# Performance work log

Measured on AMD Instinct MI355X. Metric: run time of the kernel, lower is better.

Reference implementation:

```python
import jax, jax.numpy as jnp
import numpy as np

EPS = 1e-5
K_NBR = 21   # num_neighbors + 1 (self)
PSI = 4


def _bn(x, g, b):
    # BatchNorm (training-mode forward): channel-last, normalize over all other axes
    axes = tuple(range(x.ndim - 1))
    m = jnp.mean(x, axis=axes, keepdims=True)
    v = jnp.var(x, axis=axes, keepdims=True)
    return (x - m) * jax.lax.rsqrt(v + EPS) * g + b


def setup_inputs() -> dict:
    key = jax.random.key(0)
    ks = jax.random.split(key, 16)
    B, N, Cin, Cout = 4, 2048, 64, 256
    h = Cout // 2
    w_ch = Cout // PSI
    heads = 2 * PSI - 1

    def w(k, o, i):
        return jax.random.normal(k, (o, i), dtype=jnp.float32) * (1.0 / np.sqrt(i))

    p = {}
    p['xyz'] = jax.random.normal(ks[0], (B, N, 3), dtype=jnp.float32)
    p['f'] = jax.random.normal(ks[1], (B, Cin, N), dtype=jnp.float32)
    p['W_geo'] = w(ks[2], h, 6);       p['g_geo'] = jnp.ones(h);   p['b_geo'] = jnp.zeros(h)
    p['W_feat'] = w(ks[3], h, 2 * Cin); p['g_feat'] = jnp.ones(h); p['b_feat'] = jnp.zeros(h)
    p['g_bn'] = jnp.ones(Cout); p['b_bn'] = jnp.zeros(Cout)
    p['W_q'] = w(ks[4], Cout, Cout); p['g_q'] = jnp.ones(Cout); p['b_q'] = jnp.zeros(Cout)
    p['W_k'] = w(ks[5], Cout, Cout); p['g_k'] = jnp.ones(Cout); p['b_k'] = jnp.zeros(Cout)
    p['W_v'] = w(ks[6], Cout, Cout); p['g_v'] = jnp.ones(Cout); p['b_v'] = jnp.zeros(Cout)
    p['W_fus'] = w(ks[7], Cout, heads * w_ch); p['bias_fus'] = jnp.zeros(Cout)
    p['g_fus'] = jnp.ones(Cout); p['b_fus'] = jnp.zeros(Cout)
    p['g_ln'] = jnp.ones(Cout); p['b_ln'] = jnp.zeros(Cout)
    p['W_mlp'] = w(ks[8], Cout, Cout); p['bias_mlp'] = jnp.zeros(Cout)
    return p


def reference(xyz, f, W_geo, g_geo, b_geo, W_feat, g_feat, b_feat, g_bn, b_bn,
              W_q, g_q, b_q, W_k, g_k, b_k, W_v, g_v, b_v,
              W_fus, bias_fus, g_fus, b_fus, g_ln, b_ln, W_mlp, bias_mlp):
    B, N, _ = xyz.shape
    Cout = g_bn.shape[0]
    w_ch = Cout // PSI
    d_sh = w_ch // 2
    heads = 2 * PSI - 1

    # ---- PositionFusion: KNN grouping ----
    sq = jnp.sum(xyz * xyz, axis=-1)                                   # [B,N]
    d2 = sq[:, :, None] + sq[:, None, :] - 2.0 * jnp.einsum('bnd,bmd->bnm', xyz, xyz)
    _, idx = jax.lax.top_k(-d2, K_NBR)                                 # [B,N,K]

    grouped_xyz = jax.vmap(lambda p, i: p[i])(xyz, idx)                # [B,N,K,3]
    xyz_diff = grouped_xyz - xyz[:, :, None, :]
    geo_in = jnp.concatenate(
        [jnp.broadcast_to(xyz[:, :, None, :], grouped_xyz.shape), xyz_diff], axis=-1)  # [B,N,K,6]

    ft = jnp.transpose(f, (0, 2, 1))                                   # [B,N,Cin]
    grouped_f = jax.vmap(lambda p, i: p[i])(ft, idx)                   # [B,N,K,Cin]
    feat_in = jnp.concatenate(
        [grouped_f, jnp.broadcast_to(ft[:, :, None, :], grouped_f.shape)], axis=-1)    # [B,N,K,2Cin]

    geo = jax.nn.relu(_bn(jnp.einsum('bnki,oi->bnko', geo_in, W_geo), g_geo, b_geo))
    fea = jax.nn.relu(_bn(jnp.einsum('bnki,oi->bnko', feat_in, W_feat), g_feat, b_feat))
    feature_ = jnp.max(jnp.concatenate([geo, fea], axis=-1), axis=2)   # [B,N,Cout] (maxpool over K)

    # ---- BatchNorm1d ----
    x = _bn(feature_, g_bn, b_bn)

    # ---- Shifted-channel multi-head attention ----
    q = jax.nn.relu(_bn(jnp.einsum('bnc,oc->bno', x, W_q), g_q, b_q))
    k = jax.nn.relu(_bn(jnp.einsum('bnc,oc->bno', x, W_k), g_k, b_k))
    v = jax.nn.relu(_bn(jnp.einsum('bnc,oc->bno', x, W_v), g_v, b_v))

    qh = jnp.stack([q[..., m * d_sh:m * d_sh + w_ch] for m in range(heads)], axis=1)  # [B,H,N,w]
    kh = jnp.stack([k[..., m * d_sh:m * d_sh + w_ch] for m in range(heads)], axis=1)
    vh = jnp.stack([v[..., m * d_sh:m * d_sh + w_ch] for m in range(heads)], axis=1)

    a = jax.nn.softmax(jnp.einsum('bhnc,bhmc->bhnm', qh, kh), axis=-1)  # [B,H,N,N]
    o = jnp.einsum('bhnm,bhmc->bhnc', a, vh)                            # [B,H,N,w]
    O = jnp.transpose(o, (0, 2, 1, 3)).reshape(B, N, heads * w_ch)      # channel-concat per head

    fus = jax.nn.relu(_bn(jnp.einsum('bnc,oc->bno', O, W_fus) + bias_fus, g_fus, b_fus))

    feature__ = fus + feature_                                          # residual

    # ---- LayerNorm over channels ----
    m = jnp.mean(feature__, axis=-1, keepdims=True)
    var = jnp.var(feature__, axis=-1, keepdims=True)
    y = (feature__ - m) * jax.lax.rsqrt(var + EPS) * g_ln + b_ln

    out = feature__ + (jnp.einsum('bnc,oc->bno', y, W_mlp) + bias_mlp)
    return jnp.transpose(out, (0, 2, 1))                                # [B,Cout,N] like torch
```

## Files before the change

kernel.cpp:

```cpp
#include <hip/hip_runtime.h>
#include <math.h>

#define NB    4
#define NPTS  2048
#define ROWS  (NB*NPTS)
#define CIN   64
#define COUT  256
#define KNBR  21
#define NHEADS 7
#define WCH   64
#define DSH   32
#define LOG2E 1.4426950408889634f

typedef __attribute__((ext_vector_type(8))) short short8;
typedef __attribute__((ext_vector_type(4))) float floatx4;

#if __has_builtin(__builtin_amdgcn_exp2f)
#define EXP2(x) __builtin_amdgcn_exp2f(x)
#else
#define EXP2(x) __expf((x)*0.6931471805599453f)
#endif
#if __has_builtin(__builtin_amdgcn_rcpf)
#define RCP(x) __builtin_amdgcn_rcpf(x)
#else
#define RCP(x) (1.0f/(x))
#endif

__device__ __forceinline__ ushort f2bf(float x) {
    unsigned u = __float_as_uint(x);
    u += 0x7fffu + ((u >> 16) & 1u);
    return (ushort)(u >> 16);
}

template<int N>
__device__ __forceinline__ float dpp_ror16(float x) {
    return __int_as_float(__builtin_amdgcn_update_dpp(
        0, __float_as_int(x), 0x120 | N, 0xF, 0xF, true));
}
__device__ __forceinline__ float dpp_max16(float x) {
    x = fmaxf(x, dpp_ror16<1>(x));
    x = fmaxf(x, dpp_ror16<2>(x));
    x = fmaxf(x, dpp_ror16<4>(x));
    x = fmaxf(x, dpp_ror16<8>(x));
    return x;
}
__device__ __forceinline__ float dpp_sum16(float x) {
    x += dpp_ror16<1>(x);
    x += dpp_ror16<2>(x);
    x += dpp_ror16<4>(x);
    x += dpp_ror16<8>(x);
    return x;
}

template<int CTRL, int RMASK>
__device__ __forceinline__ unsigned dpp_umin_step(unsigned x) {
    unsigned t = (unsigned)__builtin_amdgcn_update_dpp((int)x, (int)x, CTRL, RMASK, 0xF, false);
    return (t < x) ? t : x;
}
__device__ __forceinline__ unsigned wave_min_u32(unsigned x) {
    x = dpp_umin_step<0x111, 0xF>(x);
    x = dpp_umin_step<0x112, 0xF>(x);
    x = dpp_umin_step<0x114, 0xF>(x);
    x = dpp_umin_step<0x118, 0xF>(x);
    x = dpp_umin_step<0x142, 0xA>(x);
    x = dpp_umin_step<0x143, 0xC>(x);
    return (unsigned)__builtin_amdgcn_readlane((int)x, 63);
}

__global__ __launch_bounds__(256) void prep_knn(const float* __restrict__ f, const float* __restrict__ Wf,
                                                const float* __restrict__ xyz, const float* __restrict__ Wg,
                                                const float* __restrict__ W_q, const float* __restrict__ W_k,
                                                const float* __restrict__ W_v, const float* __restrict__ W_fus,
                                                float* __restrict__ X, float* __restrict__ A,
                                                ushort* __restrict__ Wb, float* __restrict__ sums,
                                                int* __restrict__ idx) {
    __shared__ float4 SXQ[2048];
    int t = threadIdx.x;
    int blk = blockIdx.x;
    if (blk < 512) {
        float* As = (float*)SXQ;
        float* Ws = As + 16*68;
        int bx = blk & 127, by = blk >> 7;
        if (by == 0 && bx < 12) sums[bx*256 + t] = 0.f;
        int gid = (by*128 + bx)*256 + t;
        for (int i = gid; i < 311296; i += 131072) {
            const float* Wsrc; int off;
            if (i < 65536)       { Wsrc = W_q;   off = i; }
            else if (i < 131072) { Wsrc = W_k;   off = i - 65536; }
            else if (i < 196608) { Wsrc = W_v;   off = i - 131072; }
            else                 { Wsrc = W_fus; off = i - 196608; }
            Wb[i] = f2bf(Wsrc[off]);
        }
        int r0 = bx * 64, n0 = by * 64;
        for (int e = t; e < 4096; e += 256) {
            int row = r0 + (e >> 6), c = n0 + (e & 63), cc = c & 127;
            float x = xyz[row*3], y = xyz[row*3+1], z = xyz[row*3+2];
            const float* w = Wg + cc*6;
            float s = (c < 128) ? ((w[3]*x + w[4]*y) + w[5]*z)
                                : (((w[0]-w[3])*x + (w[1]-w[4])*y) + (w[2]-w[5])*z);
            A[(size_t)row*256 + c] = s;
        }
        int b = r0 >> 11, nbase = r0 & 2047;
        int tx = t & 15, ty = t >> 4;
        float acc[4][4];
#pragma unroll
        for (int i = 0; i < 4; i++)
#pragma unroll
            for (int j = 0; j < 4; j++) acc[i][j] = 0.f;
        int m64 = t & 63, kg = t >> 6;
        int lk = t & 15, lm = t >> 4;
        for (int k0 = 0; k0 < 64; k0 += 16) {
#pragma unroll
            for (int p = 0; p < 4; p++) {
                int k = kg*4 + p;
                As[k*68 + m64] = f[(size_t)b*CIN*NPTS + (size_t)(k0 + k)*NPTS + nbase + m64];
            }
#pragma unroll
            for (int i2 = 0; i2 < 4; i2++) {
                int cg = n0 + lm + 16*i2;
                Ws[lk*68 + lm + 16*i2] = Wf[(size_t)(cg & 127)*128 + (cg >> 7)*64 + k0 + lk];
            }
            __syncthreads();
#pragma unroll
            for (int kq = 0; kq < 16; kq++) {
                float4 a  = *(const float4*)&As[kq*68 + 4*ty];
                float4 b4 = *(const float4*)&Ws[kq*68 + 4*tx];
                float av[4] = {a.x, a.y, a.z, a.w};
                float bv[4] = {b4.x, b4.y, b4.z, b4.w};
#pragma unroll
                for (int i = 0; i < 4; i++)
#pragma unroll
                    for (int j = 0; j < 4; j++) acc[i][j] = fmaf(av[i], bv[j], acc[i][j]);
            }
            __syncthreads();
        }
#pragma unroll
        for (int i = 0; i < 4; i++)
#pragma unroll
            for (int j = 0; j < 4; j++)
                X[(size_t)(r0 + 4*ty + i)*256 + n0 + 4*tx + j] = acc[i][j];
        return;
    }
    int kb = blk - 512;
    int b = kb >> 9;
    int g = kb & 511;
    for (int m = t; m < NPTS; m += 256) {
        float x = xyz[(size_t)b*NPTS*3 + m*3];
        float y = xyz[(size_t)b*NPTS*3 + m*3 + 1];
        float z = xyz[(size_t)b*NPTS*3 + m*3 + 2];
        SXQ[m] = make_float4(x, y, z, (x*x + y*y) + z*z);
    }
    __syncthreads();
    int w = t >> 6, lane = t & 63;
    int n = g*4 + w;
    float4 q4 = SXQ[n];
    float qx = q4.x, qy = q4.y, qz = q4.z, sqn = q4.w;
    unsigned key[32];
#pragma unroll
    for (int i = 0; i < 32; i++) {
        int m = lane + (i << 6);
        float4 p = SXQ[m];
        float dt = (qx*p.x + qy*p.y) + qz*p.z;
        float d2 = fmaxf((sqn + p.w) - 2.0f*dt, 0.f);
        key[i] = (__float_as_uint(d2) & 0xFFFFF800u) | (unsigned)m;
    }
    unsigned winkey = 0xFFFFFFFFu;
    for (int kk = 0; kk < 32; kk++) {
        unsigned lv = key[0];
#pragma unroll
        for (int i = 1; i < 32; i++) lv = (key[i] < lv) ? key[i] : lv;
        unsigned win = wave_min_u32(lv);
        if (lane == kk) winkey = win;
        unsigned widx = win & 2047u;
        int slot = (int)(widx >> 6);
        bool own = (lane == (int)(widx & 63u));
#pragma unroll
        for (int i = 0; i < 32; i++)
            if (i == slot && own) key[i] = 0xFFFFFFFFu;
    }
    double d2r;
    int mr;
    {
        double qx64 = (double)qx, qy64 = (double)qy, qz64 = (double)qz;
        double sqn64 = qx64*qx64 + qy64*qy64 + qz64*qz64;
        if (lane < 32) {
            mr = (int)(winkey & 2047u);
            float4 p = SXQ[mr];
            double x = (double)p.x, y = (double)p.y, z = (double)p.z;
            double sqm = x*x + y*y + z*z;
            double dt  = qx64*x + qy64*y + qz64*z;
            d2r = (sqn64 + sqm) - 2.0*dt;
        } else {
            d2r = INFINITY; mr = 0x7FFFFFFF;
        }
    }
#pragma unroll
    for (int k = 2; k <= 32; k <<= 1) {
#pragma unroll
        for (int j = k >> 1; j > 0; j >>= 1) {
            double od = __shfl_xor(d2r, j, 64);
            int    om = __shfl_xor(mr, j, 64);
            bool up    = ((lane & k) == 0);
            bool lower = ((lane & j) == 0);
            bool oless = (od < d2r) || (od == d2r && om < mr);
            bool keepOther = up ? (lower ? oless : !oless) : (lower ? !oless : oless);
            if (keepOther) { d2r = od; mr = om; }
        }
    }
    if (lane < KNBR)
        idx[((size_t)b*NPTS + n)*KNBR + lane] = mr;
}

__global__ __launch_bounds__(256) void stats_gf(const float* __restrict__ geoBC, const float* __restrict__ featAC,
                                                const int* __restrict__ idx, const float* __restrict__ g_geo,
                                                const float* __restrict__ g_feat,
                                                float* __restrict__ sums, float* __restrict__ xsel) {
    int c = threadIdx.x;
    int cc = c & 127;
    const float* base = (c < 128) ? geoBC : featAC;
    bool wantmax = ((c < 128) ? g_geo[cc] : g_feat[cc]) >= 0.f;
    float s = 0.f, ss = 0.f;
    int r0 = blockIdx.x * 32;
    for (int r = r0; r < r0 + 32; r++) {
        int b = r >> 11;
        float ctr = base[(size_t)r*256 + 128 + cc];
        float mx = -1e30f, mn = 1e30f;
        const int* ip = idx + (size_t)r*KNBR;
        for (int kk = 0; kk < KNBR; kk++) {
            int j = ip[kk];
            float xv = ctr + base[((size_t)(b*NPTS + j))*256 + cc];
            mx = fmaxf(mx, xv); mn = fminf(mn, xv);
            s += xv; ss += xv*xv;
        }
        xsel[(size_t)r*256 + c] = wantmax ? mx : mn;
    }
    atomicAdd(&sums[c], s);
    atomicAdd(&sums[256 + c], ss);
}

__global__ __launch_bounds__(256) void feature_maxsel(const float* __restrict__ xsel, const float* __restrict__ sums,
                                                      const float* __restrict__ g_geo, const float* __restrict__ b_geo,
                                                      const float* __restrict__ g_feat, const float* __restrict__ b_feat,
                                                      float* __restrict__ feat, float* __restrict__ sums_bn1) {
    int c = threadIdx.x;
    const float inv = 1.0f / (float)(ROWS*KNBR);
    float mean = sums[c]*inv;
    float var  = sums[256+c]*inv - mean*mean;
    float g  = (c < 128) ? g_geo[c] : g_feat[c-128];
    float bb = (c < 128) ? b_geo[c] : b_feat[c-128];
    float sc = g / sqrtf(var + 1e-5f);
    float tt = bb - mean*sc;
    float s = 0.f, ss = 0.f;
    int r0 = blockIdx.x*32;
    for (int r = r0; r < r0+32; r++) {
        size_t i = (size_t)r*256 + c;
        float y = fmaxf(fmaf(sc, xsel[i], tt), 0.f);
        feat[i] = y; s += y; ss += y*y;
    }
    atomicAdd(&sums_bn1[c], s); atomicAdd(&sums_bn1[256+c], ss);
}

__global__ __launch_bounds__(256) void gemm_qkv(const float* __restrict__ Af, const float* __restrict__ sums_in,
                                                const float* __restrict__ g_bn, const float* __restrict__ b_bn,
                                                const ushort* __restrict__ Wb,
                                                float* __restrict__ QKVF, float* __restrict__ sums) {
    __shared__ float bns[2][256];
    __shared__ float red[4][256][2];
    int t = threadIdx.x;
    int r0 = blockIdx.x * 64, g = blockIdx.y;
    int w = t >> 6, lane = t & 63;
    int r15 = lane & 15, quad = lane >> 4;
    {
        float mean = sums_in[512 + t] * (1.0f/(float)ROWS);
        float var  = sums_in[768 + t] * (1.0f/(float)ROWS) - mean*mean;
        float sc = g_bn[t] / sqrtf(var + 1e-5f);
        bns[0][t] = sc;
        bns[1][t] = b_bn[t] - mean*sc;
    }
    __syncthreads();
    short8 aq[8];
    {
        const float* ap = Af + (size_t)(r0 + 16*w + r15)*256;
#pragma unroll
        for (int kc = 0; kc < 8; kc++) {
            int k0 = 32*kc + 8*quad;
            float4 a0 = *(const float4*)&ap[k0];
            float4 a1 = *(const float4*)&ap[k0+4];
            float4 s0 = *(const float4*)&bns[0][k0];
            float4 s1 = *(const float4*)&bns[0][k0+4];
            float4 h0 = *(const float4*)&bns[1][k0];
            float4 h1 = *(const float4*)&bns[1][k0+4];
            ushort u8[8];
            u8[0] = f2bf(fmaf(s0.x, a0.x, h0.x)); u8[1] = f2bf(fmaf(s0.y, a0.y, h0.y));
            u8[2] = f2bf(fmaf(s0.z, a0.z, h0.z)); u8[3] = f2bf(fmaf(s0.w, a0.w, h0.w));
            u8[4] = f2bf(fmaf(s1.x, a1.x, h1.x)); u8[5] = f2bf(fmaf(s1.y, a1.y, h1.y));
            u8[6] = f2bf(fmaf(s1.z, a1.z, h1.z)); u8[7] = f2bf(fmaf(s1.w, a1.w, h1.w));
            aq[kc] = *(short8*)u8;
        }
    }
    floatx4 zero4 = {0.f, 0.f, 0.f, 0.f};
    floatx4 acc[16];
#pragma unroll
    for (int st = 0; st < 16; st++) acc[st] = zero4;
    const ushort* wbase = Wb + (size_t)g*65536 + (size_t)r15*256 + 8*quad;
#pragma unroll
    for (int st = 0; st < 16; st++) {
        const ushort* wp = wbase + (size_t)(16*st)*256;
#pragma unroll
        for (int kc = 0; kc < 8; kc++) {
            short8 bf = *(const short8*)(wp + 32*kc);
            acc[st] = __builtin_amdgcn_mfma_f32_16x16x32_bf16(aq[kc], bf, acc[st], 0, 0, 0);
        }
    }
#pragma unroll
    for (int st = 0; st < 16; st++) {
        float s  = (acc[st][0] + acc[st][1]) + (acc[st][2] + acc[st][3]);
        float q2 = (acc[st][0]*acc[st][0] + acc[st][1]*acc[st][1]) +
                   (acc[st][2]*acc[st][2] + acc[st][3]*acc[st][3]);
        s  += __shfl_xor(s, 16, 64);  s  += __shfl_xor(s, 32, 64);
        q2 += __shfl_xor(q2, 16, 64); q2 += __shfl_xor(q2, 32, 64);
        if (lane < 16) { red[w][16*st + r15][0] = s; red[w][16*st + r15][1] = q2; }
#pragma unroll
        for (int reg = 0; reg < 4; reg++)
            QKVF[(size_t)(r0 + 16*w + 4*quad + reg)*768 + g*256 + 16*st + r15] = acc[st][reg];
    }
    __syncthreads();
    {
        float s = red[0][t][0] + red[1][t][0] + red[2][t][0] + red[3][t][0];
        float q = red[0][t][1] + red[1][t][1] + red[2][t][1] + red[3][t][1];
        atomicAdd(&sums[1024 + g*512 + t], s);
        atomicAdd(&sums[1024 + g*512 + 256 + t], q);
    }
}

__global__ __launch_bounds__(256) void affine_qkv(const float* __restrict__ QKVF, const float* __restrict__ sums,
                                                  const float* __restrict__ g_q, const float* __restrict__ b_q,
                                                  const float* __restrict__ g_k, const float* __restrict__ b_k,
                                                  const float* __restrict__ g_v, const float* __restrict__ b_v,
                                                  ushort* __restrict__ qk, ushort* __restrict__ vt) {
    __shared__ float sts[6][256];
    __shared__ ushort tile[64][72];
    int t = threadIdx.x;
    {
        const float* gs[3] = {g_q, g_k, g_v};
        const float* bs[3] = {b_q, b_k, b_v};
#pragma unroll
        for (int g = 0; g < 3; g++) {
            float mean = sums[1024 + g*512 + t] * (1.0f/(float)ROWS);
            float var  = sums[1024 + g*512 + 256 + t] * (1.0f/(float)ROWS) - mean*mean;
            float sc = gs[g][t] / sqrtf(var + 1e-5f);
            float sh = bs[g][t] - mean*sc;
            if (g == 0) { sc *= LOG2E; sh *= LOG2E; }
            sts[2*g][t] = sc;
            sts[2*g+1][t] = sh;
        }
    }
    __syncthreads();
    int r0 = blockIdx.x * 64, c0 = blockIdx.y * 64;
    int b = r0 >> 11, nbase = r0 & 2047;
    if (c0 < 512) {
#pragma unroll
        for (int rep = 0; rep < 16; rep++) {
            int e = t + 256*rep;
            int row = e >> 6, c = e & 63;
            int col = c0 + c, g = col >> 8, cc = col & 255;
            float v = QKVF[(size_t)(r0 + row)*768 + col];
            v = fmaxf(fmaf(sts[2*g][cc], v, sts[2*g+1][cc]), 0.f);
            qk[(size_t)(r0 + row)*512 + col] = f2bf(v);
        }
    } else {
#pragma unroll
        for (int rep = 0; rep < 16; rep++) {
            int e = t + 256*rep;
            int row = e >> 6, c = e & 63;
            int col = c0 + c, cc = col & 255;
            float v = QKVF[(size_t)(r0 + row)*768 + col];
            v = fmaxf(fmaf(sts[4][cc], v, sts[5][cc]), 0.f);
            tile[c][row] = f2bf(v);
        }
        __syncthreads();
#pragma unroll
        for (int rep = 0; rep < 16; rep++) {
            int e = t + 256*rep;
            int cc = e >> 6, nn = e & 63;
            vt[((size_t)(b*256 + (c0 - 512) + cc))*2048 + nbase + nn] = tile[cc][nn];
        }
    }
}

__global__ __launch_bounds__(256) void attn2(const ushort* __restrict__ qk, const ushort* __restrict__ vt,
                                             float* __restrict__ obuf) {
    __shared__ ushort Ksh[64*72];
    __shared__ ushort Vts[64*72];
    __shared__ ushort Psh[128*72];
    int h = blockIdx.y, b = blockIdx.z;
    int r0 = blockIdx.x * 128;
    int t = threadIdx.x;
    int w = t >> 6, lane = t & 63;
    int r15 = lane & 15, quad = lane >> 4;
    size_t rowbase = (size_t)b*NPTS;
    int hoff = h*DSH;

    short8 aq[2][2];
#pragma unroll
    for (int u = 0; u < 2; u++)
#pragma unroll
        for (int s = 0; s < 2; s++)
            aq[u][s] = *(const short8*)(qk + (rowbase + r0 + 64*u + 16*w + r15)*512 + hoff + 32*s + 8*quad);

    floatx4 zero4 = {0.f, 0.f, 0.f, 0.f};
    floatx4 oacc[2][4];
    float mrun[2][4], lrun[2][4];
#pragma unroll
    for (int u = 0; u < 2; u++)
#pragma unroll
        for (int i = 0; i < 4; i++) { oacc[u][i] = zero4; mrun[u][i] = -1e30f; lrun[u][i] = 0.f; }

    for (int m0 = 0; m0 < NPTS; m0 += 64) {
#pragma unroll
        for (int rep = 0; rep < 2; rep++) {
            int e = t + 256*rep;
            int rr = e >> 3, c = e & 7;
            *(uint4*)&Ksh[rr*72 + 8*c] =
                *(const uint4*)(qk + (rowbase + m0 + rr)*512 + 256 + hoff + 8*c);
            *(uint4*)&Vts[rr*72 + 8*c] =
                *(const uint4*)(vt + ((size_t)(b*256 + hoff + rr))*2048 + m0 + 8*c);
        }
        __syncthreads();

        floatx4 sacc[2][4];
#pragma unroll
        for (int u = 0; u < 2; u++)
#pragma unroll
            for (int tt = 0; tt < 4; tt++) sacc[u][tt] = zero4;
#pragma unroll
        for (int tt = 0; tt < 4; tt++) {
            int key = 16*tt + r15;
#pragma unroll
            for (int s = 0; s < 2; s++) {
                short8 kf = *(const short8*)&Ksh[key*72 + 32*s + 8*quad];
#pragma unroll
                for (int u = 0; u < 2; u++)
                    sacc[u][tt] = __builtin_amdgcn_mfma_f32_16x16x32_bf16(aq[u][s], kf, sacc[u][tt], 0, 0, 0);
            }
        }

        float pm[2][4][4];
#pragma unroll
        for (int u = 0; u < 2; u++)
#pragma unroll
            for (int reg = 0; reg < 4; reg++) {
                float rmax = fmaxf(fmaxf(sacc[u][0][reg], sacc[u][1][reg]),
                                   fmaxf(sacc[u][2][reg], sacc[u][3][reg]));
                rmax = dpp_max16(rmax);
                float mnew = fmaxf(mrun[u][reg], rmax);
                float alpha = EXP2(mrun[u][reg] - mnew);
                float rs = 0.f;
#pragma unroll
                for (int tt = 0; tt < 4; tt++) {
                    float p = EXP2(sacc[u][tt][reg] - mnew);
                    pm[u][tt][reg] = p; rs += p;
                }
                rs = dpp_sum16(rs);
                lrun[u][reg] = lrun[u][reg]*alpha + rs;
                mrun[u][reg] = mnew;
#pragma unroll
                for (int td = 0; td < 4; td++) oacc[u][td][reg] *= alpha;
            }

#pragma unroll
        for (int u = 0; u < 2; u++)
#pragma unroll
            for (int reg = 0; reg < 4; reg++) {
                int row = 64*u + 16*w + 4*quad + reg;
#pragma unroll
                for (int tt = 0; tt < 4; tt++)
                    Psh[row*72 + 16*tt + r15] = f2bf(pm[u][tt][reg]);
            }
        __syncthreads();

#pragma unroll
        for (int s = 0; s < 2; s++) {
            short8 pf[2];
#pragma unroll
            for (int u = 0; u < 2; u++)
                pf[u] = *(const short8*)&Psh[(64*u + 16*w + r15)*72 + 32*s + 8*quad];
#pragma unroll
            for (int td = 0; td < 4; td++) {
                short8 vf = *(const short8*)&Vts[(16*td + r15)*72 + 32*s + 8*quad];
#pragma unroll
                for (int u = 0; u < 2; u++)
                    oacc[u][td] = __builtin_amdgcn_mfma_f32_16x16x32_bf16(pf[u], vf, oacc[u][td], 0, 0, 0);
            }
        }
        __syncthreads();
    }

#pragma unroll
    for (int u = 0; u < 2; u++)
#pragma unroll
        for (int reg = 0; reg < 4; reg++) {
            int grow = r0 + 64*u + 16*w + 4*quad + reg;
            float invl = RCP(lrun[u][reg]);
#pragma unroll
            for (int td = 0; td < 4; td++)
                obuf[(rowbase + grow)*(size_t)(NHEADS*WCH) + h*WCH + 16*td + r15] = oacc[u][td][reg]*invl;
        }
}

__global__ __launch_bounds__(256) void gemm_fus(const float* __restrict__ OBUF, const ushort* __restrict__ Wb,
                                                const float* __restrict__ bias, float* __restrict__ C,
                                                float* __restrict__ sums) {
    __shared__ float red[4][128][2];
    int t = threadIdx.x;
    int r0 = blockIdx.x * 64, n0 = blockIdx.y * 128;
    int w = t >> 6, lane = t & 63;
    int r15 = lane & 15, quad = lane >> 4;
    int arow = 16*w + r15;
    short8 aq[14];
    {
        const float* p0 = OBUF + (size_t)(r0 + arow)*448;
#pragma unroll
        for (int kc = 0; kc < 14; kc++) {
            int k0 = 32*kc + 8*quad;
            float4 x0 = *(const float4*)&p0[k0];
            float4 y0 = *(const float4*)&p0[k0+4];
            ushort u8[8];
            u8[0] = f2bf(x0.x); u8[1] = f2bf(x0.y);
            u8[2] = f2bf(x0.z); u8[3] = f2bf(x0.w);
            u8[4] = f2bf(y0.x); u8[5] = f2bf(y0.y);
            u8[6] = f2bf(y0.z); u8[7] = f2bf(y0.w);
            aq[kc] = *(short8*)u8;
        }
    }
    floatx4 zero4 = {0.f, 0.f, 0.f, 0.f};
    floatx4 acc[8];
#pragma unroll
    for (int st = 0; st < 8; st++) acc[st] = zero4;
    const ushort* wbase = Wb + 196608 + (size_t)(n0 + r15)*448 + 8*quad;
#pragma unroll
    for (int st = 0; st < 8; st++) {
        const ushort* wp = wbase + (size_t)(16*st)*448;
#pragma unroll
        for (int kc = 0; kc < 14; kc++) {
            short8 bf = *(const short8*)(wp + 32*kc);
            acc[st] = __builtin_amdgcn_mfma_f32_16x16x32_bf16(aq[kc], bf, acc[st], 0, 0, 0);
        }
    }
#pragma unroll
    for (int st = 0; st < 8; st++) {
        int col = n0 + 16*st + r15;
        float bi = bias[col];
        float v0 = acc[st][0] + bi, v1 = acc[st][1] + bi, v2 = acc[st][2] + bi, v3 = acc[st][3] + bi;
        float s  = (v0 + v1) + (v2 + v3);
        float q2 = (v0*v0 + v1*v1) + (v2*v2 + v3*v3);
        s  += __shfl_xor(s, 16, 64);  s  += __shfl_xor(s, 32, 64);
        q2 += __shfl_xor(q2, 16, 64); q2 += __shfl_xor(q2, 32, 64);
        if (lane < 16) { red[w][16*st + r15][0] = s; red[w][16*st + r15][1] = q2; }
        C[(size_t)(r0 + 16*w + 4*quad + 0)*256 + col] = v0;
        C[(size_t)(r0 + 16*w + 4*quad + 1)*256 + col] = v1;
        C[(size_t)(r0 + 16*w + 4*quad + 2)*256 + col] = v2;
        C[(size_t)(r0 + 16*w + 4*quad + 3)*256 + col] = v3;
    }
    __syncthreads();
    {
        int col = t >> 1, which = t & 1;
        float v = red[0][col][which] + red[1][col][which] + red[2][col][which] + red[3][col][which];
        atomicAdd(&sums[2560 + which*256 + n0 + col], v);
    }
}

__global__ __launch_bounds__(256) void gemm_mlp_ln(const float* __restrict__ FUSP, const float* __restrict__ A,
                                                   const float* __restrict__ sums,
                                                   const float* __restrict__ g_fus, const float* __restrict__ b_fus,
                                                   const float* __restrict__ g_ln, const float* __restrict__ b_ln,
                                                   const float* __restrict__ W, const float* __restrict__ bias,
                                                   float* __restrict__ outp) {
    __shared__ float Ys[256][68];
    __shared__ float FFs[64][65];
    __shared__ float Ws[16][68];
    __shared__ float tr[64][65];
    __shared__ float SC[256], SH[256], GL[256], BL[256];
    int t = threadIdx.x;
    int r0 = blockIdx.x*64, n0 = blockIdx.y*64;
    {
        float mean0 = sums[2560 + t] * (1.0f/(float)ROWS);
        float var0  = sums[2560 + 256 + t] * (1.0f/(float)ROWS) - mean0*mean0;
        float sc = g_fus[t] / sqrtf(var0 + 1e-5f);
        SC[t] = sc; SH[t] = b_fus[t] - mean0*sc;
        GL[t] = g_ln[t]; BL[t] = b_ln[t];
    }
    __syncthreads();
    int row = t >> 2, seg = t & 3;
    size_t rb = (size_t)(r0 + row)*256;
    float4 vv[16];
    float s = 0.f, ss = 0.f;
#pragma unroll
    for (int j = 0; j < 16; j++) {
        int c = seg*64 + 4*j;
        float4 fp = *(const float4*)&FUSP[rb + c];
        float4 fe = *(const float4*)&A[rb + c];
        float4 sc4 = *(const float4*)&SC[c];
        float4 sh4 = *(const float4*)&SH[c];
        float4 v;
        v.x = fmaxf(fmaf(sc4.x, fp.x, sh4.x), 0.f) + fe.x;
        v.y = fmaxf(fmaf(sc4.y, fp.y, sh4.y), 0.f) + fe.y;
        v.z = fmaxf(fmaf(sc4.z, fp.z, sh4.z), 0.f) + fe.z;
        v.w = fmaxf(fmaf(sc4.w, fp.w, sh4.w), 0.f) + fe.w;
        vv[j] = v;
        s  += (v.x + v.y) + (v.z + v.w);
        ss += (v.x*v.x + v.y*v.y) + (v.z*v.z + v.w*v.w);
        if (seg == blockIdx.y) *(float4*)&FFs[row][4*j] = v;
    }
    s  += __shfl_xor(s, 1, 64);  s  += __shfl_xor(s, 2, 64);
    ss += __shfl_xor(ss, 1, 64); ss += __shfl_xor(ss, 2, 64);
    float mean = s * (1.f/256.f);
    float var  = ss * (1.f/256.f) - mean*mean;
    float rin  = 1.f/sqrtf(var + 1e-5f);
#pragma unroll
    for (int j = 0; j < 16; j++) {
        int c = seg*64 + 4*j;
        float4 gl = *(const float4*)&GL[c];
        float4 bl = *(const float4*)&BL[c];
        float4 v = vv[j];
        Ys[c+0][row] = (v.x - mean)*rin*gl.x + bl.x;
        Ys[c+1][row] = (v.y - mean)*rin*gl.y + bl.y;
        Ys[c+2][row] = (v.z - mean)*rin*gl.z + bl.z;
        Ys[c+3][row] = (v.w - mean)*rin*gl.w + bl.w;
    }
    __syncthreads();
    int tx = t & 15, ty = t >> 4;
    int lk = t & 15, lm = t >> 4;
    float acc[4][4];
#pragma unroll
    for (int i = 0; i < 4; i++)
#pragma unroll
        for (int j = 0; j < 4; j++) acc[i][j] = 0.f;
    for (int k0 = 0; k0 < 256; k0 += 16) {
#pragma unroll
        for (int i2 = 0; i2 < 4; i2++)
            Ws[lk][lm + 16*i2] = W[(size_t)(n0 + lm + 16*i2)*256 + k0 + lk];
        __syncthreads();
#pragma unroll
        for (int kq = 0; kq < 16; kq++) {
            float4 a  = *(const float4*)&Ys[k0 + kq][4*ty];
            float4 b4 = *(const float4*)&Ws[kq][4*tx];
            float av[4] = {a.x, a.y, a.z, a.w};
            float bv[4] = {b4.x, b4.y, b4.z, b4.w};
#pragma unroll
            for (int i = 0; i < 4; i++)
#pragma unroll
                for (int j = 0; j < 4; j++) acc[i][j] = fmaf(av[i], bv[j], acc[i][j]);
        }
        __syncthreads();
    }
#pragma unroll
    for (int i = 0; i < 4; i++)
#pragma unroll
        for (int j = 0; j < 4; j++) {
            float v = acc[i][j] + bias[n0 + 4*tx + j] + FFs[4*ty + i][4*tx + j];
            tr[4*tx + j][4*ty + i] = v;
        }
    __syncthreads();
    int b = r0 >> 11, nbase = r0 & 2047;
#pragma unroll
    for (int rep = 0; rep < 16; rep++) {
        int e = t + 256*rep;
        int cl = e >> 6, nl = e & 63;
        outp[((size_t)(b*256 + n0 + cl))*2048 + nbase + nl] = tr[cl][nl];
    }
}

extern "C" void kernel_launch(void* const* d_in, const int* in_sizes, int n_in,
                              void* d_out, int out_size, void* d_ws, size_t ws_size,
                              hipStream_t stream) {
    const float* xyz    = (const float*)d_in[0];
    const float* f      = (const float*)d_in[1];
    const float* W_geo  = (const float*)d_in[2];
    const float* g_geo  = (const float*)d_in[3];
    const float* b_geo  = (const float*)d_in[4];
    const float* W_feat = (const float*)d_in[5];
    const float* g_feat = (const float*)d_in[6];
    const float* b_feat = (const float*)d_in[7];
    const float* g_bn   = (const float*)d_in[8];
    const float* b_bn   = (const float*)d_in[9];
    const float* W_q    = (const float*)d_in[10];
    const float* g_q    = (const float*)d_in[11];
    const float* b_q    = (const float*)d_in[12];
    const float* W_k    = (const float*)d_in[13];
    const float* g_k    = (const float*)d_in[14];
    const float* b_k    = (const float*)d_in[15];
    const float* W_v    = (const float*)d_in[16];
    const float* g_v    = (const float*)d_in[17];
    const float* b_v    = (const float*)d_in[18];
    const float* W_fus  = (const float*)d_in[19];
    const float* bias_fus = (const float*)d_in[20];
    const float* g_fus  = (const float*)d_in[21];
    const float* b_fus  = (const float*)d_in[22];
    const float* g_ln   = (const float*)d_in[23];
    const float* b_ln   = (const float*)d_in[24];
    const float* W_mlp  = (const float*)d_in[25];
    const float* bias_mlp = (const float*)d_in[26];

    float* ws = (float*)d_ws;
    const size_t MBF = 262144;
    float* SUMS  = ws;
    int*   IDX   = (int*)(ws + 16384);
    float* A     = ws + 1*MBF;
    float* X     = ws + 9*MBF;
    ushort* QK16 = (ushort*)(ws + 9*MBF);
    float* FUSP  = ws + 9*MBF;
    float* CSEL  = ws + 17*MBF;
    float* QKVF  = ws + 17*MBF;
    float* OBUF  = ws + 17*MBF;
    ushort* VT16 = (ushort*)(ws + 45*MBF);
    ushort* WB16 = (ushort*)(ws + 49*MBF);

    prep_knn<<<2560, 256, 0, stream>>>(f, W_feat, xyz, W_geo, W_q, W_k, W_v, W_fus,
                                       X, A, WB16, SUMS, IDX);
    stats_gf<<<256, 256, 0, stream>>>(A, X, IDX, g_geo, g_feat, SUMS, CSEL);
    feature_maxsel<<<256, 256, 0, stream>>>(CSEL, SUMS, g_geo, b_geo, g_feat, b_feat, A, SUMS + 512);
    gemm_qkv<<<dim3(128, 3), 256, 0, stream>>>(A, SUMS, g_bn, b_bn, WB16, QKVF, SUMS);
    affine_qkv<<<dim3(128, 12), 256, 0, stream>>>(QKVF, SUMS, g_q, b_q, g_k, b_k, g_v, b_v, QK16, VT16);
    attn2<<<dim3(NPTS/128, NHEADS, NB), 256, 0, stream>>>(QK16, VT16, OBUF);
    gemm_fus<<<dim3(128, 2), 256, 0, stream>>>(OBUF, WB16, bias_fus, FUSP, SUMS);
    gemm_mlp_ln<<<dim3(128, 4), 256, 0, stream>>>(FUSP, A, SUMS, g_fus, b_fus, g_ln, b_ln,
                                                  W_mlp, bias_mlp, (float*)d_out);
}
```

Baseline: 434.3 us.

## Split attention work across eight waves and drop intra-tile P barrier

```diff
diff --git a/kernel.cpp b/kernel.cpp
--- a/kernel.cpp
+++ b/kernel.cpp
@@ -388,7 +388,7 @@
     }
 }
 
-__global__ __launch_bounds__(256) void attn2(const ushort* __restrict__ qk, const ushort* __restrict__ vt,
+__global__ __launch_bounds__(512) void attn2(const ushort* __restrict__ qk, const ushort* __restrict__ vt,
                                              float* __restrict__ obuf) {
     __shared__ ushort Ksh[64*72];
     __shared__ ushort Vts[64*72];
@@ -401,26 +401,20 @@
     size_t rowbase = (size_t)b*NPTS;
     int hoff = h*DSH;
 
-    short8 aq[2][2];
-#pragma unroll
-    for (int u = 0; u < 2; u++)
-#pragma unroll
-        for (int s = 0; s < 2; s++)
-            aq[u][s] = *(const short8*)(qk + (rowbase + r0 + 64*u + 16*w + r15)*512 + hoff + 32*s + 8*quad);
+    short8 aq[2];
+#pragma unroll
+    for (int s = 0; s < 2; s++)
+        aq[s] = *(const short8*)(qk + (rowbase + r0 + 16*w + r15)*512 + hoff + 32*s + 8*quad);
 
     floatx4 zero4 = {0.f, 0.f, 0.f, 0.f};
-    floatx4 oacc[2][4];
-    float mrun[2][4], lrun[2][4];
-#pragma unroll
-    for (int u = 0; u < 2; u++)
-#pragma unroll
-        for (int i = 0; i < 4; i++) { oacc[u][i] = zero4; mrun[u][i] = -1e30f; lrun[u][i] = 0.f; }
+    floatx4 oacc[4];
+    float mrun[4], lrun[4];
+#pragma unroll
+    for (int i = 0; i < 4; i++) { oacc[i] = zero4; mrun[i] = -1e30f; lrun[i] = 0.f; }
 
     for (int m0 = 0; m0 < NPTS; m0 += 64) {
-#pragma unroll
-        for (int rep = 0; rep < 2; rep++) {
-            int e = t + 256*rep;
-            int rr = e >> 3, c = e & 7;
+        {
+            int rr = t >> 3, c = t & 7;
             *(uint4*)&Ksh[rr*72 + 8*c] =
                 *(const uint4*)(qk + (rowbase + m0 + rr)*512 + 256 + hoff + 8*c);
             *(uint4*)&Vts[rr*72 + 8*c] =
@@ -428,84 +422,68 @@
         }
         __syncthreads();
 
-        floatx4 sacc[2][4];
-#pragma unroll
-        for (int u = 0; u < 2; u++)
-#pragma unroll
-            for (int tt = 0; tt < 4; tt++) sacc[u][tt] = zero4;
+        floatx4 sacc[4];
+#pragma unroll
+        for (int tt = 0; tt < 4; tt++) sacc[tt] = zero4;
 #pragma unroll
         for (int tt = 0; tt < 4; tt++) {
             int key = 16*tt + r15;
 #pragma unroll
             for (int s = 0; s < 2; s++) {
                 short8 kf = *(const short8*)&Ksh[key*72 + 32*s + 8*quad];
-#pragma unroll
-                for (int u = 0; u < 2; u++)
-                    sacc[u][tt] = __builtin_amdgcn_mfma_f32_16x16x32_bf16(aq[u][s], kf, sacc[u][tt], 0, 0, 0);
+                sacc[tt] = __builtin_amdgcn_mfma_f32_16x16x32_bf16(aq[s], kf, sacc[tt], 0, 0, 0);
             }
         }
 
-        float pm[2][4][4];
-#pragma unroll
-        for (int u = 0; u < 2; u++)
-#pragma unroll
-            for (int reg = 0; reg < 4; reg++) {
-                float rmax = fmaxf(fmaxf(sacc[u][0][reg], sacc[u][1][reg]),
-                                   fmaxf(sacc[u][2][reg], sacc[u][3][reg]));
-                rmax = dpp_max16(rmax);
-                float mnew = fmaxf(mrun[u][reg], rmax);
-                float alpha = EXP2(mrun[u][reg] - mnew);
-                float rs = 0.f;
-#pragma unroll
-                for (int tt = 0; tt < 4; tt++) {
-                    float p = EXP2(sacc[u][tt][reg] - mnew);
-                    pm[u][tt][reg] = p; rs += p;
-                }
-                rs = dpp_sum16(rs);
-                lrun[u][reg] = lrun[u][reg]*alpha + rs;
-                mrun[u][reg] = mnew;
-#pragma unroll
-                for (int td = 0; td < 4; td++) oacc[u][td][reg] *= alpha;
+        float pm[4][4];
+#pragma unroll
+        for (int reg = 0; reg < 4; reg++) {
+            float rmax = fmaxf(fmaxf(sacc[0][reg], sacc[1][reg]),
+                               fmaxf(sacc[2][reg], sacc[3][reg]));
+            rmax = dpp_max16(rmax);
+            float mnew = fmaxf(mrun[reg], rmax);
+            float alpha = EXP2(mrun[reg] - mnew);
+            float rs = 0.f;
+#pragma unroll
+            for (int tt = 0; tt < 4; tt++) {
+                float p = EXP2(sacc[tt][reg] - mnew);
+                pm[tt][reg] = p; rs += p;
             }
-
-#pragma unroll
-        for (int u = 0; u < 2; u++)
-#pragma unroll
-            for (int reg = 0; reg < 4; reg++) {
-                int row = 64*u + 16*w + 4*quad + reg;
-#pragma unroll
-                for (int tt = 0; tt < 4; tt++)
-                    Psh[row*72 + 16*tt + r15] = f2bf(pm[u][tt][reg]);
-            }
-        __syncthreads();
+            rs = dpp_sum16(rs);
+            lrun[reg] = lrun[reg]*alpha + rs;
+            mrun[reg] = mnew;
+#pragma unroll
+            for (int td = 0; td < 4; td++) oacc[td][reg] *= alpha;
+        }
+
+#pragma unroll
+        for (int reg = 0; reg < 4; reg++) {
+            int row = 16*w + 4*quad + reg;
+#pragma unroll
+            for (int tt = 0; tt < 4; tt++)
+                Psh[row*72 + 16*tt + r15] = f2bf(pm[tt][reg]);
+        }
 
 #pragma unroll
         for (int s = 0; s < 2; s++) {
-            short8 pf[2];
-#pragma unroll
-            for (int u = 0; u < 2; u++)
-                pf[u] = *(const short8*)&Psh[(64*u + 16*w + r15)*72 + 32*s + 8*quad];
+            short8 pf = *(const short8*)&Psh[(16*w + r15)*72 + 32*s + 8*quad];
 #pragma unroll
             for (int td = 0; td < 4; td++) {
                 short8 vf = *(const short8*)&Vts[(16*td + r15)*72 + 32*s + 8*quad];
-#pragma unroll
-                for (int u = 0; u < 2; u++)
-                    oacc[u][td] = __builtin_amdgcn_mfma_f32_16x16x32_bf16(pf[u], vf, oacc[u][td], 0, 0, 0);
+                oacc[td] = __builtin_amdgcn_mfma_f32_16x16x32_bf16(pf, vf, oacc[td], 0, 0, 0);
             }
         }
         __syncthreads();
     }
 
 #pragma unroll
-    for (int u = 0; u < 2; u++)
-#pragma unroll
-        for (int reg = 0; reg < 4; reg++) {
-            int grow = r0 + 64*u + 16*w + 4*quad + reg;
-            float invl = RCP(lrun[u][reg]);
-#pragma unroll
-            for (int td = 0; td < 4; td++)
-                obuf[(rowbase + grow)*(size_t)(NHEADS*WCH) + h*WCH + 16*td + r15] = oacc[u][td][reg]*invl;
-        }
+    for (int reg = 0; reg < 4; reg++) {
+        int grow = r0 + 16*w + 4*quad + reg;
+        float invl = RCP(lrun[reg]);
+#pragma unroll
+        for (int td = 0; td < 4; td++)
+            obuf[(rowbase + grow)*(size_t)(NHEADS*WCH) + h*WCH + 16*td + r15] = oacc[td][reg]*invl;
+    }
 }
 
 __global__ __launch_bounds__(256) void gemm_fus(const float* __restrict__ OBUF, const ushort* __restrict__ Wb,
@@ -722,7 +700,7 @@
     feature_maxsel<<<256, 256, 0, stream>>>(CSEL, SUMS, g_geo, b_geo, g_feat, b_feat, A, SUMS + 512);
     gemm_qkv<<<dim3(128, 3), 256, 0, stream>>>(A, SUMS, g_bn, b_bn, WB16, QKVF, SUMS);
     affine_qkv<<<dim3(128, 12), 256, 0, stream>>>(QKVF, SUMS, g_q, b_q, g_k, b_k, g_v, b_v, QK16, VT16);
-    attn2<<<dim3(NPTS/128, NHEADS, NB), 256, 0, stream>>>(QK16, VT16, OBUF);
+    attn2<<<dim3(NPTS/128, NHEADS, NB), 512, 0, stream>>>(QK16, VT16, OBUF);
     gemm_fus<<<dim3(128, 2), 256, 0, stream>>>(OBUF, WB16, bias_fus, FUSP, SUMS);
     gemm_mlp_ln<<<dim3(128, 4), 256, 0, stream>>>(FUSP, A, SUMS, g_fus, b_fus, g_ln, b_ln,
                                                   W_mlp, bias_mlp, (float*)d_out);
```

Measured after the change: 421.1 us. -3.0%, faster.
